# Kernel tuning notes

Measured on AMD Instinct MI355X. Metric: run time of the kernel, lower is better.

The kernel has to match this reference:

```python
import jax, jax.numpy as jnp
import numpy as np


def setup_inputs() -> dict:
    key = jax.random.key(0)
    pred = jax.random.normal(key, (16, 4, 768, 768), dtype=jnp.float32)
    return {"pred": pred}


def _largest_cc(mask):
    """Largest 4-connected component of a 2D boolean mask, as float32 0/1.

    Equivalent to scipy.ndimage.label (default 4-connectivity) followed by
    keeping the largest label. Uses min-label flood propagation: each
    foreground pixel starts with its raster index; iterated neighbor-min
    converges so every pixel holds its component's minimum pixel index
    (the 'root'). Ties in size resolve to the smallest root, which matches
    scipy's label-order tie-breaking (labels assigned in raster order).
    """
    H, W = mask.shape
    HW = H * W
    idx = jnp.arange(HW, dtype=jnp.int32).reshape(H, W)
    BIG = jnp.int32(HW)  # sentinel for background
    lbl0 = jnp.where(mask, idx, BIG)

    def body(carry):
        lbl, _ = carry
        p = jnp.pad(lbl, 1, constant_values=HW)
        nb = jnp.minimum(jnp.minimum(p[:-2, 1:-1], p[2:, 1:-1]),
                         jnp.minimum(p[1:-1, :-2], p[1:-1, 2:]))
        new = jnp.where(mask, jnp.minimum(lbl, nb), BIG)
        return new, jnp.any(new != lbl)

    lbl, _ = jax.lax.while_loop(lambda c: c[1], body, (lbl0, jnp.any(mask)))

    # component sizes keyed by root pixel index; background bucket = HW
    sizes = jax.ops.segment_sum(mask.ravel().astype(jnp.int32), lbl.ravel(),
                                num_segments=HW + 1)
    sizes = sizes.at[HW].set(0)
    root = jnp.argmax(sizes).astype(jnp.int32)
    return ((lbl == root) & mask).astype(jnp.float32)


def reference(pred):
    B, C, H, W = pred.shape
    labels = jnp.argmax(pred, axis=1)  # [B, H, W]
    cls = jnp.arange(1, C, dtype=labels.dtype)
    masks = labels[:, None, :, :] == cls[None, :, None, None]  # [B, C-1, H, W]
    comp = jax.vmap(_largest_cc)(masks.reshape(-1, H, W)).reshape(B, C - 1, H, W)
    bg = 1.0 - jnp.clip(comp.sum(axis=1), 0.0, 1.0)  # channel 0
    return jnp.concatenate([bg[:, None], comp], axis=1)
```

## Files before the change

### kernel.cpp

```cpp
#include <hip/hip_runtime.h>
#include <stdint.h>

#define BB 16
#define CC 4
#define HH 768
#define WW 768
#define HW (HH * WW)
#define NPIX (BB * HW)
#define NIMG (BB * (CC - 1))
#define BEST_STRIDE 16

#define TS 64
#define TPI (WW / TS)
#define TILES_PER_IMG (TPI * TPI)
#define TPIX (TS * TS)
#define CCL_TPB 256

typedef unsigned long long ull;


__device__ __forceinline__ int find_root(int* P, int i) {
    int p = P[i];
    while (p != i) {
        int gp = P[p];
        P[i] = gp;
        i = p;
        p = gp;
    }
    return i;
}

__device__ __forceinline__ void merge(int* P, int a, int b) {
    a = find_root(P, a);
    b = find_root(P, b);
    while (a != b) {
        if (a < b) { int t = a; a = b; b = t; }
        int old = atomicCAS(&P[a], a, b);
        if (old == a) return;
        a = find_root(P, old);
        b = find_root(P, b);
    }
}


__device__ __forceinline__ int lfind(int* P, int i) {
    int p = P[i];
    while (p != i) {
        int gp = P[p];
        P[i] = gp;
        i = p;
        p = gp;
    }
    return i;
}

__device__ __forceinline__ void lmerge(int* P, int a, int b) {
    a = lfind(P, a);
    b = lfind(P, b);
    while (a != b) {
        if (a < b) { int t = a; a = b; b = t; }
        int old = atomicCAS(&P[a], a, b);
        if (old == a) return;
        a = lfind(P, old);
        b = lfind(P, b);
    }
}

__device__ __forceinline__ ull umax64(ull a, ull b) { return a > b ? a : b; }


__global__ __launch_bounds__(CCL_TPB) void k_tile_ccl(
        const float* __restrict__ pred,
        uint8_t* __restrict__ labels,
        int* __restrict__ parent,
        uint32_t* __restrict__ counts,
        ull* __restrict__ best) {
    __shared__ __align__(16) int sp[TPIX];
    __shared__ __align__(16) uint8_t slab[TPIX];

    if (blockIdx.x == 0) {
        for (int i = threadIdx.x; i < NIMG * BEST_STRIDE; i += CCL_TPB) best[i] = 0ull;
    }

    const int tid = (int)threadIdx.x;
    const int img = blockIdx.x / TILES_PER_IMG;
    const int tile = blockIdx.x % TILES_PER_IMG;
    const int tr = (tile / TPI) * TS;
    const int tc = (tile % TPI) * TS;
    const float* pb = pred + (size_t)img * CC * HW;
    const int imgbase = img * HW;

    for (int k = 0; k < TPIX; k += CCL_TPB * 4) {
        int li = k + tid * 4;
        int gi = (tr + (li >> 6)) * WW + tc + (li & 63);
        float4 v0 = *(const float4*)&pb[gi];
        float4 v1 = *(const float4*)&pb[gi + HW];
        float4 v2 = *(const float4*)&pb[gi + 2 * HW];
        float4 v3 = *(const float4*)&pb[gi + 3 * HW];
        const float* a0 = &v0.x; const float* a1 = &v1.x;
        const float* a2 = &v2.x; const float* a3 = &v3.x;
        uchar4 lout;
        uint8_t* lj = &lout.x;
        #pragma unroll
        for (int j = 0; j < 4; ++j) {
            int lab = 0;
            float bv = a0[j];
            if (a1[j] > bv) { bv = a1[j]; lab = 1; }
            if (a2[j] > bv) { bv = a2[j]; lab = 2; }
            if (a3[j] > bv) { bv = a3[j]; lab = 3; }
            lj[j] = (uint8_t)lab;
        }
        *(uchar4*)&slab[li] = lout;
        *(uchar4*)&labels[imgbase + gi] = lout;
    }
    __syncthreads();

    const int c = tid & 63;

    #pragma unroll 1
    for (int it = 0; it < TPIX / CCL_TPB; ++it) {
        int li = it * CCL_TPB + tid;
        int lab = slab[li];
        int labL = __shfl_up(lab, 1, 64);
        bool isStart = lab && (c == 0 || labL != lab);
        ull mask = __ballot(isStart);
        int v = li;
        if (lab) {
            ull mle = mask & (~0ull >> (63 - c));
            v = (li & ~63) + (63 - __clzll(mle));
        }
        sp[li] = v;
    }
    __syncthreads();

    #pragma unroll 1
    for (int it = 0; it < TPIX / CCL_TPB; ++it) {
        int li = it * CCL_TPB + tid;
        int lab = slab[li];
        int labU = (li >= TS) ? (int)slab[li - TS] : 0;
        int labL = __shfl_up(lab, 1, 64);
        int labUL = __shfl_up(labU, 1, 64);
        if (lab && labU == lab) {
            if (c == 0 || !(labL == lab && labUL == lab))
                lmerge(sp, li, li - TS);
        }
    }
    __syncthreads();

    #pragma unroll 1
    for (int it = 0; it < TPIX / CCL_TPB; ++it) {
        int li = it * CCL_TPB + tid;
        int lab = slab[li];
        int labL = __shfl_up(lab, 1, 64);
        bool isStart = lab && (c == 0 || labL != lab);
        bool isEnd = lab && (c == 63 || (int)slab[li + 1] != lab);
        ull endmask = __ballot(isEnd);
        if (lab) {
            int p = sp[li] & 0xFFFF;
            if (p != li) {
                int q0 = sp[p] & 0xFFFF;
                while (q0 != p) { p = q0; q0 = sp[p] & 0xFFFF; }
                sp[li] = p;
            }
            if (isStart) {
                ull mge = endmask & (~0ull << c);
                int epos = __ffsll((long long)mge) - 1;
                int runlen = epos - c + 1;
                atomicAdd((unsigned int*)&sp[p], (unsigned int)runlen << 16);
            }
        }
    }
    __syncthreads();

    for (int k = 0; k < TPIX; k += CCL_TPB * 4) {
        int li = k + tid * 4;
        int gi = imgbase + (tr + (li >> 6)) * WW + tc + (li & 63);
        uchar4 lv = *(const uchar4*)&slab[li];
        int4 sv = *(const int4*)&sp[li];
        const uint8_t* lj = &lv.x;
        const int* sj = &sv.x;
        int4 pout; uint4 cout;
        int* pj = &pout.x; uint32_t* cj = &cout.x;
        #pragma unroll
        for (int j = 0; j < 4; ++j) {
            int root = sj[j] & 0xFFFF;
            if (lj[j]) {
                pj[j] = imgbase + (tr + (root >> 6)) * WW + tc + (root & 63);
                cj[j] = (root == li + j) ? ((uint32_t)sj[j] >> 16) : 0u;
            } else {
                pj[j] = -1;
                cj[j] = 0u;
            }
        }
        *(int4*)&parent[gi] = pout;
        *(uint4*)&counts[gi] = cout;
    }
}

#define VEDGES ((TPI - 1) * HH)
#define EDGES_PER_IMG (2 * (TPI - 1) * HH)
__global__ void k_border_merge(const uint8_t* __restrict__ labels, int* parent) {
    int t = blockIdx.x * blockDim.x + threadIdx.x;
    if (t >= BB * EDGES_PER_IMG) return;
    int img = t / EDGES_PER_IMG;
    int e = t % EDGES_PER_IMG;
    int a, b;
    if (e < VEDGES) {
        int j = e / HH, r = e % HH;
        int c = j * TS + TS - 1;
        a = r * WW + c;
        b = a + 1;
    } else {
        e -= VEDGES;
        int j = e / WW, c = e % WW;
        int r = j * TS + TS - 1;
        a = r * WW + c;
        b = a + WW;
    }
    int ga = img * HW + a, gb = img * HW + b;
    uint8_t la = labels[ga];
    if (la && labels[gb] == la) merge(parent, ga, gb);
}

__global__ void k_compress(int* __restrict__ parent, uint32_t* __restrict__ counts) {
    int q = blockIdx.x * blockDim.x + threadIdx.x;
    if (q >= NPIX / 4) return;
    int t = q * 4;
    uint4 cv = *(const uint4*)&counts[t];
    if (!(cv.x | cv.y | cv.z | cv.w)) return;
    uint32_t cs[4] = {cv.x, cv.y, cv.z, cv.w};
    #pragma unroll
    for (int j = 0; j < 4; ++j) {
        if (!cs[j]) continue;
        int i = t + j;
        int g = parent[i];
        if (g == i) continue;
        while (true) { int pg = parent[g]; if (pg == g) break; g = pg; }
        parent[i] = g;
        atomicAdd(&counts[g], cs[j]);
        counts[i] = 0;
    }
}

#define BEST_BLK_PER_IMG 144
#define BEST_TPB 256
#define BEST_PIX_PER_BLK (HW / BEST_BLK_PER_IMG)
__global__ void k_best(const uint8_t* __restrict__ labels,
                       const uint32_t* __restrict__ counts,
                       ull* __restrict__ best) {
    __shared__ ull sw[(BEST_TPB / 64) * 3];
    int img = blockIdx.x / BEST_BLK_PER_IMG;
    int chunk = blockIdx.x % BEST_BLK_PER_IMG;
    int base = img * HW + chunk * BEST_PIX_PER_BLK;

    ull l0 = 0, l1 = 0, l2 = 0;
    for (int k = 0; k < BEST_PIX_PER_BLK; k += BEST_TPB * 4) {
        int t = base + k + (int)threadIdx.x * 4;
        uint4 cv = *(const uint4*)&counts[t];
        if (cv.x | cv.y | cv.z | cv.w) {
            uchar4 lv = *(const uchar4*)&labels[t];
            uint32_t cs[4] = {cv.x, cv.y, cv.z, cv.w};
            uint8_t ls[4] = {lv.x, lv.y, lv.z, lv.w};
            #pragma unroll
            for (int j = 0; j < 4; ++j) {
                if (cs[j]) {
                    int cc = (int)ls[j] - 1;
                    ull key = ((ull)cs[j] << 32) | (ull)(~(uint32_t)(t + j));
                    if (cc == 0) l0 = umax64(l0, key);
                    else if (cc == 1) l1 = umax64(l1, key);
                    else l2 = umax64(l2, key);
                }
            }
        }
    }
    #pragma unroll
    for (int m = 1; m < 64; m <<= 1) {
        l0 = umax64(l0, __shfl_xor(l0, m, 64));
        l1 = umax64(l1, __shfl_xor(l1, m, 64));
        l2 = umax64(l2, __shfl_xor(l2, m, 64));
    }
    int lane = threadIdx.x & 63;
    int wid = threadIdx.x >> 6;
    if (lane == 0) { sw[wid * 3 + 0] = l0; sw[wid * 3 + 1] = l1; sw[wid * 3 + 2] = l2; }
    __syncthreads();
    if (threadIdx.x < 3) {
        ull m = 0;
        for (int w = 0; w < BEST_TPB / 64; ++w) m = umax64(m, sw[w * 3 + threadIdx.x]);
        if (m) atomicMax(&best[(img * 3 + (int)threadIdx.x) * BEST_STRIDE], m);
    }
}

__global__ void k_output(const uint8_t* __restrict__ labels,
                         const int* __restrict__ parent,
                         const ull* __restrict__ best,
                         float* __restrict__ out) {
    int q = blockIdx.x * blockDim.x + threadIdx.x;
    if (q >= NPIX / 4) return;
    int t = q * 4;
    int b = t / HW;
    int i = t - b * HW;
    uchar4 lv = *(const uchar4*)&labels[t];
    int4 pv = *(const int4*)&parent[t];
    int root[3];
    root[0] = (int)(~(uint32_t)best[(b * 3 + 0) * BEST_STRIDE]);
    root[1] = (int)(~(uint32_t)best[(b * 3 + 1) * BEST_STRIDE]);
    root[2] = (int)(~(uint32_t)best[(b * 3 + 2) * BEST_STRIDE]);

    uint8_t ls[4] = {lv.x, lv.y, lv.z, lv.w};
    int ps[4] = {pv.x, pv.y, pv.z, pv.w};
    float fg[4];
    #pragma unroll
    for (int j = 0; j < 4; ++j) {
        int g = -1;
        if (ps[j] >= 0) g = parent[ps[j]];
        fg[j] = (ls[j] && g == root[ls[j] - 1]) ? 1.0f : 0.0f;
    }

    float4 o0, o1, o2, o3;
    float* c0 = &o0.x; float* c1 = &o1.x; float* c2 = &o2.x; float* c3 = &o3.x;
    #pragma unroll
    for (int j = 0; j < 4; ++j) {
        c0[j] = 1.0f - fg[j];
        c1[j] = (ls[j] == 1) ? fg[j] : 0.0f;
        c2[j] = (ls[j] == 2) ? fg[j] : 0.0f;
        c3[j] = (ls[j] == 3) ? fg[j] : 0.0f;
    }
    float* o = out + (size_t)b * CC * HW + i;
    *(float4*)&o[0] = o0;
    *(float4*)&o[HW] = o1;
    *(float4*)&o[2 * HW] = o2;
    *(float4*)&o[3 * HW] = o3;
}


extern "C" void kernel_launch(void* const* d_in, const int* in_sizes, int n_in,
                              void* d_out, int out_size, void* d_ws, size_t ws_size,
                              hipStream_t stream) {
    const float* pred = (const float*)d_in[0];
    float* out = (float*)d_out;

    uint8_t* labels = (uint8_t*)d_ws;
    int* parent = (int*)((char*)d_ws + NPIX);
    ull* best = (ull*)((char*)d_ws + NPIX + (size_t)NPIX * 4);
    uint32_t* counts = (uint32_t*)d_out;

    const int TPB = 256;

    k_tile_ccl<<<BB * TILES_PER_IMG, CCL_TPB, 0, stream>>>(pred, labels, parent, counts, best);
    k_border_merge<<<(BB * EDGES_PER_IMG + TPB - 1) / TPB, TPB, 0, stream>>>(labels, parent);
    k_compress<<<(NPIX / 4 + TPB - 1) / TPB, TPB, 0, stream>>>(parent, counts);
    k_best<<<BB * BEST_BLK_PER_IMG, BEST_TPB, 0, stream>>>(labels, counts, best);
    k_output<<<(NPIX / 4 + TPB - 1) / TPB, TPB, 0, stream>>>(labels, parent, best, out);
}
```

Measured before the change: 154.2 us.

## Give each wavefront a 16-row strip for fused run init and vertical merging

```diff
diff --git a/kernel.cpp b/kernel.cpp
--- a/kernel.cpp
+++ b/kernel.cpp
@@ -15,6 +15,7 @@
 #define TILES_PER_IMG (TPI * TPI)
 #define TPIX (TS * TS)
 #define CCL_TPB 256
+#define STRIP 16
 
 typedef unsigned long long ull;
 
@@ -67,6 +68,11 @@
 }
 
 __device__ __forceinline__ ull umax64(ull a, ull b) { return a > b ? a : b; }
+
+__device__ __forceinline__ void lds_fence() {
+    asm volatile("s_waitcnt lgkmcnt(0)" ::: "memory");
+    __builtin_amdgcn_sched_barrier(0);
+}
 
 
 __global__ __launch_bounds__(CCL_TPB) void k_tile_ccl(
@@ -115,41 +121,61 @@
     }
     __syncthreads();
 
-    const int c = tid & 63;
+    const int w = tid >> 6;
+    const int lane = tid & 63;
+
+    {
+        int prevLab = 0, prevV = 0;
+        #pragma unroll 1
+        for (int r = 0; r < STRIP; ++r) {
+            int row = (w << 4) + r;
+            int li = (row << 6) + lane;
+            int lab = slab[li];
+            int labL = __shfl_up(lab, 1, 64);
+            bool isStart = lab && (lane == 0 || labL != lab);
+            ull mask = __ballot(isStart);
+            int v = li;
+            if (lab) {
+                ull mle = mask & (~0ull >> (63 - lane));
+                v = (row << 6) + (63 - __clzll(mle));
+            }
+            sp[li] = v;
+            lds_fence();
+            if (r > 0) {
+                int labUL = __shfl_up(prevLab, 1, 64);
+                if (lab && prevLab == lab) {
+                    if (lane == 0 || !(labL == lab && labUL == lab))
+                        lmerge(sp, v, prevV);
+                }
+            }
+            prevLab = lab;
+            prevV = v;
+        }
+    }
+    __syncthreads();
+
+    if (tid < 64 * 3) {
+        int row = ((tid >> 6) + 1) << 4;
+        int c = tid & 63;
+        int li = (row << 6) + c;
+        int lab = slab[li];
+        int labU = slab[li - TS];
+        if (lab && labU == lab) {
+            bool seg = true;
+            if (c > 0) {
+                int labL = slab[li - 1];
+                int labUL = slab[li - TS - 1];
+                seg = !(labL == lab && labUL == lab);
+            }
+            if (seg) lmerge(sp, li, li - TS);
+        }
+    }
+    __syncthreads();
 
     #pragma unroll 1
     for (int it = 0; it < TPIX / CCL_TPB; ++it) {
         int li = it * CCL_TPB + tid;
-        int lab = slab[li];
-        int labL = __shfl_up(lab, 1, 64);
-        bool isStart = lab && (c == 0 || labL != lab);
-        ull mask = __ballot(isStart);
-        int v = li;
-        if (lab) {
-            ull mle = mask & (~0ull >> (63 - c));
-            v = (li & ~63) + (63 - __clzll(mle));
-        }
-        sp[li] = v;
-    }
-    __syncthreads();
-
-    #pragma unroll 1
-    for (int it = 0; it < TPIX / CCL_TPB; ++it) {
-        int li = it * CCL_TPB + tid;
-        int lab = slab[li];
-        int labU = (li >= TS) ? (int)slab[li - TS] : 0;
-        int labL = __shfl_up(lab, 1, 64);
-        int labUL = __shfl_up(labU, 1, 64);
-        if (lab && labU == lab) {
-            if (c == 0 || !(labL == lab && labUL == lab))
-                lmerge(sp, li, li - TS);
-        }
-    }
-    __syncthreads();
-
-    #pragma unroll 1
-    for (int it = 0; it < TPIX / CCL_TPB; ++it) {
-        int li = it * CCL_TPB + tid;
+        int c = tid & 63;
         int lab = slab[li];
         int labL = __shfl_up(lab, 1, 64);
         bool isStart = lab && (c == 0 || labL != lab);
```

Result: faster. 150.1 us (-2.6%).
